# Kernel optimization log

Measured on AMD Instinct MI355X. Metric: run time of the kernel, lower is better.

The kernel has to match this reference:

```python
import jax, jax.numpy as jnp
import numpy as np

D_MODEL, N_LEVELS, N_HEADS, N_POINTS = 256, 3, 8, 2
HEAD_DIM = D_MODEL // N_HEADS
SPATIAL_SHAPES = np.array([[100, 100], [50, 50], [25, 25]], dtype=np.int32)
LEN_IN = int((SPATIAL_SHAPES[:, 0] * SPATIAL_SHAPES[:, 1]).sum())  # 13125
BS, NQ = 16, 900


def setup_inputs() -> dict:
    key = jax.random.key(0)
    ks = jax.random.split(key, 12)
    s = 1.0 / np.sqrt(D_MODEL)
    return {
        "query": jax.random.normal(ks[0], (BS, NQ, N_LEVELS, D_MODEL), jnp.float32),
        "reference_points": jax.random.uniform(ks[1], (BS, NQ, N_LEVELS, 2), jnp.float32),
        "input_flatten": jax.random.normal(ks[2], (BS, LEN_IN, D_MODEL), jnp.float32),
        "input_spatial_shapes": jnp.asarray(SPATIAL_SHAPES),
        "W_value": jax.random.normal(ks[3], (D_MODEL, D_MODEL), jnp.float32) * s,
        "b_value": jnp.zeros((D_MODEL,), jnp.float32),
        "W_off": jax.random.normal(ks[4], (D_MODEL, N_HEADS * N_LEVELS * N_POINTS * 2), jnp.float32) * s * 0.1,
        "b_off": jax.random.normal(ks[5], (N_HEADS * N_LEVELS * N_POINTS * 2,), jnp.float32) * 0.5,
        "W_attn": jax.random.normal(ks[6], (D_MODEL, N_HEADS * N_LEVELS * N_POINTS), jnp.float32) * s,
        "b_attn": jnp.zeros((N_HEADS * N_LEVELS * N_POINTS,), jnp.float32),
        "W_out": jax.random.normal(ks[7], (D_MODEL, D_MODEL), jnp.float32) * s,
        "b_out": jnp.zeros((D_MODEL,), jnp.float32),
    }


def _bilinear_sample(v, loc, H, W):
    """v: (bs, nh, H*W, hd); loc in [0,1]: (bs, nh, N, 2). Zero-pad out of range."""
    hd = v.shape[-1]
    x = loc[..., 0] * W - 0.5
    y = loc[..., 1] * H - 0.5
    x0 = jnp.floor(x)
    y0 = jnp.floor(y)
    out = jnp.zeros(x.shape + (hd,), v.dtype)
    for dx in (0, 1):
        for dy in (0, 1):
            xi = x0 + dx
            yi = y0 + dy
            wgt = (1.0 - jnp.abs(x - xi)) * (1.0 - jnp.abs(y - yi))
            valid = (xi >= 0) & (xi <= W - 1) & (yi >= 0) & (yi <= H - 1)
            xi_c = jnp.clip(xi, 0, W - 1).astype(jnp.int32)
            yi_c = jnp.clip(yi, 0, H - 1).astype(jnp.int32)
            idx = yi_c * W + xi_c  # (bs, nh, N)
            idx = jnp.broadcast_to(idx[..., None], idx.shape + (hd,))
            g = jnp.take_along_axis(v, idx, axis=2)  # (bs, nh, N, hd)
            out = out + g * (wgt * valid.astype(wgt.dtype))[..., None]
    return out


def reference(query, reference_points, input_flatten, input_spatial_shapes,
              W_value, b_value, W_off, b_off, W_attn, b_attn, W_out, b_out):
    bs, nq, fl, _ = query.shape
    shapes = np.asarray(input_spatial_shapes)  # static pyramid shapes

    # value projection: (bs, Len, nh, hd)
    value = (input_flatten @ W_value + b_value).reshape(bs, -1, N_HEADS, HEAD_DIM)

    # sampling offsets: (bs, nq, fl, nh, nl, np, 2)
    offsets = (query @ W_off + b_off).reshape(bs, nq, fl, N_HEADS, N_LEVELS, N_POINTS, 2)
    # attention weights softmax over (nl*np): (bs, nq, fl, nh, nl, np)
    attn = (query @ W_attn + b_attn).reshape(bs, nq, fl, N_HEADS, N_LEVELS * N_POINTS)
    attn = jax.nn.softmax(attn, axis=-1).reshape(bs, nq, fl, N_HEADS, N_LEVELS, N_POINTS)

    # normalized sampling locations: ref + offset / (W_l, H_l)
    normalizer = jnp.asarray(shapes[:, ::-1], jnp.float32)  # (nl, 2) = (W, H)
    loc = reference_points[:, :, :, None, None, None, :] + offsets / normalizer[None, None, None, None, :, None, :]

    splits = np.cumsum([h * w for h, w in shapes])[:-1]
    value_list = jnp.split(value, splits, axis=1)

    out = jnp.zeros((bs, N_HEADS, nq, fl, HEAD_DIM), value.dtype)
    for lvl, (H, W) in enumerate(shapes):
        H, W = int(H), int(W)
        v = jnp.transpose(value_list[lvl], (0, 2, 1, 3))  # (bs, nh, H*W, hd)
        loc_l = jnp.transpose(loc[:, :, :, :, lvl], (0, 3, 1, 2, 4, 5))  # (bs, nh, nq, fl, np, 2)
        loc_flat = loc_l.reshape(bs, N_HEADS, nq * fl * N_POINTS, 2)
        sampled = _bilinear_sample(v, loc_flat, H, W).reshape(bs, N_HEADS, nq, fl, N_POINTS, HEAD_DIM)
        w = jnp.transpose(attn[:, :, :, :, lvl], (0, 3, 1, 2, 4))  # (bs, nh, nq, fl, np)
        out = out + jnp.einsum("bhqfpd,bhqfp->bhqfd", sampled, w)

    out = jnp.transpose(out, (0, 2, 3, 1, 4)).reshape(bs, nq, fl, D_MODEL)
    return out @ W_out + b_out
```

## Files before the change

kernel.cpp:

```cpp
#include <hip/hip_runtime.h>
#include <math.h>

#define D_MODEL   256
#define N_HEADS   8
#define HEAD_DIM  32
#define N_LEVELS  3
#define N_POINTS  2
#define BS        16
#define NQ        900
#define LEN_IN    13125
#define M_Q       (BS * NQ * N_LEVELS)
#define M_V       (BS * LEN_IN)

typedef _Float16 f16x8 __attribute__((ext_vector_type(8)));
typedef _Float16 f16x4 __attribute__((ext_vector_type(4)));
typedef float f32x4 __attribute__((ext_vector_type(4)));

__global__ __launch_bounds__(256) void convert_weight_kernel(
    const float* __restrict__ W, _Float16* __restrict__ Wth,
    _Float16* __restrict__ Wtl, int N, int Npad) {
  const int idx = blockIdx.x * 256 + threadIdx.x;
  if (idx >= Npad * 256) return;
  const int n = idx >> 8;
  const int k = idx & 255;
  const float v = (n < N) ? W[(size_t)k * N + n] : 0.0f;
  const _Float16 h = (_Float16)v;
  Wth[idx] = h;
  Wtl[idx] = (_Float16)(v - (float)h);
}

template <int BN>
__global__ __launch_bounds__(256) void gemm_mfma_f16x3_kernel(
    const float* __restrict__ A, const _Float16* __restrict__ Bth,
    const _Float16* __restrict__ Btl, const float* __restrict__ bias,
    float* __restrict__ C, int M, int N) {
  constexpr int K = 256;
  constexpr int BK = 32;
  constexpr int FC = BN / 64;
  __shared__ _Float16 Ah[64][40];
  __shared__ _Float16 Al[64][40];
  __shared__ _Float16 Bh[BN][40];
  __shared__ _Float16 Bl[BN][40];

  const int tid = threadIdx.x;
  const int wid = tid >> 6;
  const int lane = tid & 63;
  const int bm = blockIdx.x * 64;

  const int a_row0 = tid >> 3;
  const int a_k4 = (tid & 7) * 4;

  f32x4 acc[4][FC];
#pragma unroll
  for (int fr = 0; fr < 4; ++fr)
#pragma unroll
    for (int fc = 0; fc < FC; ++fc) acc[fr][fc] = (f32x4)0.0f;

  const int khi = (lane >> 4) * 8;
  const int rsel = lane & 15;

  for (int k0 = 0; k0 < K; k0 += BK) {
#pragma unroll
    for (int it = 0; it < 2; ++it) {
      const int row = a_row0 + it * 32;
      float4 v = make_float4(0.f, 0.f, 0.f, 0.f);
      if (bm + row < M)
        v = *reinterpret_cast<const float4*>(
            &A[(size_t)(bm + row) * K + k0 + a_k4]);
      f16x4 h, l;
      h[0] = (_Float16)v.x; l[0] = (_Float16)(v.x - (float)h[0]);
      h[1] = (_Float16)v.y; l[1] = (_Float16)(v.y - (float)h[1]);
      h[2] = (_Float16)v.z; l[2] = (_Float16)(v.z - (float)h[2]);
      h[3] = (_Float16)v.w; l[3] = (_Float16)(v.w - (float)h[3]);
      *reinterpret_cast<f16x4*>(&Ah[row][a_k4]) = h;
      *reinterpret_cast<f16x4*>(&Al[row][a_k4]) = l;
    }
#pragma unroll
    for (int it = 0; it < BN / 64; ++it) {
      const int i = tid + 256 * it;
      const int col = i >> 2;
      const int k8 = (i & 3) * 8;
      *reinterpret_cast<f16x8*>(&Bh[col][k8]) =
          *reinterpret_cast<const f16x8*>(&Bth[(size_t)col * K + k0 + k8]);
      *reinterpret_cast<f16x8*>(&Bl[col][k8]) =
          *reinterpret_cast<const f16x8*>(&Btl[(size_t)col * K + k0 + k8]);
    }
    __syncthreads();

    f16x8 afh[4], afl[4], bfh[FC], bfl[FC];
#pragma unroll
    for (int fr = 0; fr < 4; ++fr) {
      afh[fr] = *reinterpret_cast<const f16x8*>(&Ah[fr * 16 + rsel][khi]);
      afl[fr] = *reinterpret_cast<const f16x8*>(&Al[fr * 16 + rsel][khi]);
    }
#pragma unroll
    for (int fc = 0; fc < FC; ++fc) {
      const int c = wid * (BN / 4) + fc * 16 + rsel;
      bfh[fc] = *reinterpret_cast<const f16x8*>(&Bh[c][khi]);
      bfl[fc] = *reinterpret_cast<const f16x8*>(&Bl[c][khi]);
    }
#pragma unroll
    for (int fr = 0; fr < 4; ++fr)
#pragma unroll
      for (int fc = 0; fc < FC; ++fc) {
        acc[fr][fc] = __builtin_amdgcn_mfma_f32_16x16x32_f16(
            afh[fr], bfh[fc], acc[fr][fc], 0, 0, 0);
        acc[fr][fc] = __builtin_amdgcn_mfma_f32_16x16x32_f16(
            afh[fr], bfl[fc], acc[fr][fc], 0, 0, 0);
        acc[fr][fc] = __builtin_amdgcn_mfma_f32_16x16x32_f16(
            afl[fr], bfh[fc], acc[fr][fc], 0, 0, 0);
      }
    __syncthreads();
  }

#pragma unroll
  for (int fr = 0; fr < 4; ++fr) {
#pragma unroll
    for (int i = 0; i < 4; ++i) {
      const int row = bm + fr * 16 + (lane >> 4) * 4 + i;
      if (row >= M) continue;
#pragma unroll
      for (int fc = 0; fc < FC; ++fc) {
        const int col = wid * (BN / 4) + fc * 16 + rsel;
        if (col < N)
          C[(size_t)row * N + col] = acc[fr][fc][i] + bias[col];
      }
    }
  }
}

__global__ __launch_bounds__(256) void sample_kernel(
    const float* __restrict__ value, const float* __restrict__ refpts,
    const float* __restrict__ offs, const float* __restrict__ attn,
    float* __restrict__ out_mid) {
  const int row = blockIdx.x;
  const int tid = threadIdx.x;
  const int h = tid >> 5;
  const int d = tid & 31;
  const int b = row / (NQ * N_LEVELS);

  const int LVL_W[3] = {100, 50, 25};
  const int LVL_H[3] = {100, 50, 25};
  const int LVL_BASE[3] = {0, 10000, 12500};

  const float* off_p  = offs + (size_t)row * 96 + h * 12;
  const float* attn_p = attn + (size_t)row * 48 + h * 6;

  float aw[6];
  float mx = -INFINITY;
#pragma unroll
  for (int j = 0; j < 6; ++j) {
    aw[j] = attn_p[j];
    mx = fmaxf(mx, aw[j]);
  }
  float ssum = 0.f;
#pragma unroll
  for (int j = 0; j < 6; ++j) {
    aw[j] = expf(aw[j] - mx);
    ssum += aw[j];
  }
  const float rs = 1.0f / ssum;

  const float rx = refpts[(size_t)row * 2 + 0];
  const float ry = refpts[(size_t)row * 2 + 1];

  const float* vbase = value + (size_t)b * LEN_IN * 256 + h * 32 + d;
  float acc = 0.f;

#pragma unroll
  for (int l = 0; l < N_LEVELS; ++l) {
    const int W = LVL_W[l], base = LVL_BASE[l];
    const float fW = (float)LVL_W[l], fH = (float)LVL_H[l];
#pragma unroll
    for (int p = 0; p < N_POINTS; ++p) {
      const float ox = off_p[(l * 2 + p) * 2 + 0];
      const float oy = off_p[(l * 2 + p) * 2 + 1];
      const float x = (rx + ox / fW) * fW - 0.5f;
      const float y = (ry + oy / fH) * fH - 0.5f;
      const float x0 = floorf(x);
      const float y0 = floorf(y);
      const float wa = aw[l * 2 + p] * rs;
#pragma unroll
      for (int dy = 0; dy < 2; ++dy) {
#pragma unroll
        for (int dx = 0; dx < 2; ++dx) {
          const float xi = x0 + (float)dx;
          const float yi = y0 + (float)dy;
          const float wgt = (1.0f - fabsf(x - xi)) * (1.0f - fabsf(y - yi));
          const bool valid = (xi >= 0.f) && (xi <= fW - 1.f) &&
                             (yi >= 0.f) && (yi <= fH - 1.f);
          const int xic = (int)fminf(fmaxf(xi, 0.f), fW - 1.f);
          const int yic = (int)fminf(fmaxf(yi, 0.f), fH - 1.f);
          const int pos = base + yic * W + xic;
          const float g = vbase[(size_t)pos * 256];
          acc = fmaf(g, valid ? wgt * wa : 0.0f, acc);
        }
      }
    }
  }
  out_mid[(size_t)row * 256 + tid] = acc;
}

extern "C" void kernel_launch(void* const* d_in, const int* in_sizes, int n_in,
                              void* d_out, int out_size, void* d_ws,
                              size_t ws_size, hipStream_t stream) {
  const float* query   = (const float*)d_in[0];
  const float* refpts  = (const float*)d_in[1];
  const float* in_flat = (const float*)d_in[2];
  const float* W_value = (const float*)d_in[4];
  const float* b_value = (const float*)d_in[5];
  const float* W_off   = (const float*)d_in[6];
  const float* b_off   = (const float*)d_in[7];
  const float* W_attn  = (const float*)d_in[8];
  const float* b_attn  = (const float*)d_in[9];
  const float* W_out   = (const float*)d_in[10];
  const float* b_out   = (const float*)d_in[11];
  float* out = (float*)d_out;

  char* ws = (char*)d_ws;
  float* value   = (float*)ws; ws += (size_t)M_V * 256 * sizeof(float);
  float* out_mid = (float*)ws; ws += (size_t)M_Q * 256 * sizeof(float);
  float* offs    = (float*)ws; ws += (size_t)M_Q * 96 * sizeof(float);
  float* attn    = (float*)ws; ws += (size_t)M_Q * 48 * sizeof(float);
  _Float16* Wvh = (_Float16*)ws; ws += 256 * 256 * sizeof(_Float16);
  _Float16* Wvl = (_Float16*)ws; ws += 256 * 256 * sizeof(_Float16);
  _Float16* Woh = (_Float16*)ws; ws += 256 * 256 * sizeof(_Float16);
  _Float16* Wol = (_Float16*)ws; ws += 256 * 256 * sizeof(_Float16);
  _Float16* Wfh = (_Float16*)ws; ws += 128 * 256 * sizeof(_Float16);
  _Float16* Wfl = (_Float16*)ws; ws += 128 * 256 * sizeof(_Float16);
  _Float16* Wah = (_Float16*)ws; ws += 128 * 256 * sizeof(_Float16);
  _Float16* Wal = (_Float16*)ws; ws += 128 * 256 * sizeof(_Float16);

  const dim3 blk(256);

  convert_weight_kernel<<<dim3(256), blk, 0, stream>>>(W_value, Wvh, Wvl, 256, 256);
  convert_weight_kernel<<<dim3(256), blk, 0, stream>>>(W_out,   Woh, Wol, 256, 256);
  convert_weight_kernel<<<dim3(128), blk, 0, stream>>>(W_off,   Wfh, Wfl,  96, 128);
  convert_weight_kernel<<<dim3(128), blk, 0, stream>>>(W_attn,  Wah, Wal,  48, 128);

  gemm_mfma_f16x3_kernel<256>
      <<<dim3((M_V + 63) / 64), blk, 0, stream>>>(
          in_flat, Wvh, Wvl, b_value, value, M_V, 256);

  gemm_mfma_f16x3_kernel<128>
      <<<dim3((M_Q + 63) / 64), blk, 0, stream>>>(
          query, Wfh, Wfl, b_off, offs, M_Q, 96);

  gemm_mfma_f16x3_kernel<128>
      <<<dim3((M_Q + 63) / 64), blk, 0, stream>>>(
          query, Wah, Wal, b_attn, attn, M_Q, 48);

  sample_kernel<<<dim3(M_Q), blk, 0, stream>>>(value, refpts, offs, attn,
                                               out_mid);

  gemm_mfma_f16x3_kernel<256>
      <<<dim3((M_Q + 63) / 64), blk, 0, stream>>>(
          out_mid, Woh, Wol, b_out, out, M_Q, 256);
}
```

Baseline: 807.8 us.

## Double-buffer A tiles, read B fragments from global, fuse offset/attn GEMMs

```diff
diff --git a/kernel.cpp b/kernel.cpp
--- a/kernel.cpp
+++ b/kernel.cpp
@@ -11,6 +11,8 @@
 #define LEN_IN    13125
 #define M_Q       (BS * NQ * N_LEVELS)
 #define M_V       (BS * LEN_IN)
+#define NCAT      144
+#define NCATP     192
 
 typedef _Float16 f16x8 __attribute__((ext_vector_type(8)));
 typedef _Float16 f16x4 __attribute__((ext_vector_type(4)));
@@ -29,26 +31,50 @@
   Wtl[idx] = (_Float16)(v - (float)h);
 }
 
-template <int BN>
-__global__ __launch_bounds__(256) void gemm_mfma_f16x3_kernel(
+__global__ __launch_bounds__(256) void convert_cat_kernel(
+    const float* __restrict__ Woff, const float* __restrict__ Wattn,
+    const float* __restrict__ boff, const float* __restrict__ battn,
+    _Float16* __restrict__ Wth, _Float16* __restrict__ Wtl,
+    float* __restrict__ bcat) {
+  const int idx = blockIdx.x * 256 + threadIdx.x;
+  if (idx >= NCATP * 256) return;
+  const int n = idx >> 8;
+  const int k = idx & 255;
+  float v = 0.0f;
+  if (n < 96) v = Woff[(size_t)k * 96 + n];
+  else if (n < NCAT) v = Wattn[(size_t)k * 48 + (n - 96)];
+  const _Float16 h = (_Float16)v;
+  Wth[idx] = h;
+  Wtl[idx] = (_Float16)(v - (float)h);
+  if (idx < NCAT) bcat[idx] = (idx < 96) ? boff[idx] : battn[idx - 96];
+}
+
+template <int FC>
+__global__ __launch_bounds__(256) void gemm2_kernel(
     const float* __restrict__ A, const _Float16* __restrict__ Bth,
     const _Float16* __restrict__ Btl, const float* __restrict__ bias,
     float* __restrict__ C, int M, int N) {
   constexpr int K = 256;
-  constexpr int BK = 32;
-  constexpr int FC = BN / 64;
-  __shared__ _Float16 Ah[64][40];
-  __shared__ _Float16 Al[64][40];
-  __shared__ _Float16 Bh[BN][40];
-  __shared__ _Float16 Bl[BN][40];
+  constexpr int LDA = 40;
+  __shared__ _Float16 Ah[2][64][LDA];
+  __shared__ _Float16 Al[2][64][LDA];
 
   const int tid = threadIdx.x;
   const int wid = tid >> 6;
   const int lane = tid & 63;
   const int bm = blockIdx.x * 64;
-
-  const int a_row0 = tid >> 3;
-  const int a_k4 = (tid & 7) * 4;
+  const int rsel = lane & 15;
+  const int khi = (lane >> 4) * 8;
+
+  const int arow = tid >> 3;
+  const int ak = (tid & 7) * 4;
+  const bool g0 = (bm + arow) < M;
+  const bool g1 = (bm + arow + 32) < M;
+  const float* ap0 = A + (size_t)(bm + arow) * K + ak;
+  const float* ap1 = ap0 + (size_t)32 * K;
+
+  const _Float16* bhp = Bth + (size_t)(wid * FC * 16 + rsel) * K + khi;
+  const _Float16* blp = Btl + (size_t)(wid * FC * 16 + rsel) * K + khi;
 
   f32x4 acc[4][FC];
 #pragma unroll
@@ -56,83 +82,110 @@
 #pragma unroll
     for (int fc = 0; fc < FC; ++fc) acc[fr][fc] = (f32x4)0.0f;
 
-  const int khi = (lane >> 4) * 8;
-  const int rsel = lane & 15;
-
-  for (int k0 = 0; k0 < K; k0 += BK) {
-#pragma unroll
-    for (int it = 0; it < 2; ++it) {
-      const int row = a_row0 + it * 32;
-      float4 v = make_float4(0.f, 0.f, 0.f, 0.f);
-      if (bm + row < M)
-        v = *reinterpret_cast<const float4*>(
-            &A[(size_t)(bm + row) * K + k0 + a_k4]);
-      f16x4 h, l;
-      h[0] = (_Float16)v.x; l[0] = (_Float16)(v.x - (float)h[0]);
-      h[1] = (_Float16)v.y; l[1] = (_Float16)(v.y - (float)h[1]);
-      h[2] = (_Float16)v.z; l[2] = (_Float16)(v.z - (float)h[2]);
-      h[3] = (_Float16)v.w; l[3] = (_Float16)(v.w - (float)h[3]);
-      *reinterpret_cast<f16x4*>(&Ah[row][a_k4]) = h;
-      *reinterpret_cast<f16x4*>(&Al[row][a_k4]) = l;
-    }
-#pragma unroll
-    for (int it = 0; it < BN / 64; ++it) {
-      const int i = tid + 256 * it;
-      const int col = i >> 2;
-      const int k8 = (i & 3) * 8;
-      *reinterpret_cast<f16x8*>(&Bh[col][k8]) =
-          *reinterpret_cast<const f16x8*>(&Bth[(size_t)col * K + k0 + k8]);
-      *reinterpret_cast<f16x8*>(&Bl[col][k8]) =
-          *reinterpret_cast<const f16x8*>(&Btl[(size_t)col * K + k0 + k8]);
-    }
-    __syncthreads();
-
-    f16x8 afh[4], afl[4], bfh[FC], bfl[FC];
+  const float4 z4 = make_float4(0.f, 0.f, 0.f, 0.f);
+
+  float4 a0 = g0 ? *reinterpret_cast<const float4*>(ap0) : z4;
+  float4 a1 = g1 ? *reinterpret_cast<const float4*>(ap1) : z4;
+  f16x8 bh[FC], bl[FC];
+#pragma unroll
+  for (int fc = 0; fc < FC; ++fc) {
+    bh[fc] = *reinterpret_cast<const f16x8*>(bhp + (size_t)fc * 16 * K);
+    bl[fc] = *reinterpret_cast<const f16x8*>(blp + (size_t)fc * 16 * K);
+  }
+  {
+    f16x4 h0, l0, h1, l1;
+    h0[0] = (_Float16)a0.x; l0[0] = (_Float16)(a0.x - (float)h0[0]);
+    h0[1] = (_Float16)a0.y; l0[1] = (_Float16)(a0.y - (float)h0[1]);
+    h0[2] = (_Float16)a0.z; l0[2] = (_Float16)(a0.z - (float)h0[2]);
+    h0[3] = (_Float16)a0.w; l0[3] = (_Float16)(a0.w - (float)h0[3]);
+    h1[0] = (_Float16)a1.x; l1[0] = (_Float16)(a1.x - (float)h1[0]);
+    h1[1] = (_Float16)a1.y; l1[1] = (_Float16)(a1.y - (float)h1[1]);
+    h1[2] = (_Float16)a1.z; l1[2] = (_Float16)(a1.z - (float)h1[2]);
+    h1[3] = (_Float16)a1.w; l1[3] = (_Float16)(a1.w - (float)h1[3]);
+    *reinterpret_cast<f16x4*>(&Ah[0][arow][ak]) = h0;
+    *reinterpret_cast<f16x4*>(&Al[0][arow][ak]) = l0;
+    *reinterpret_cast<f16x4*>(&Ah[0][arow + 32][ak]) = h1;
+    *reinterpret_cast<f16x4*>(&Al[0][arow + 32][ak]) = l1;
+  }
+  __syncthreads();
+
+#pragma unroll 2
+  for (int s = 0; s < 8; ++s) {
+    const int cur = s & 1;
+    float4 na0 = z4, na1 = z4;
+    f16x8 nbh[FC], nbl[FC];
+    if (s < 7) {
+      na0 = g0 ? *reinterpret_cast<const float4*>(ap0 + (s + 1) * 32) : z4;
+      na1 = g1 ? *reinterpret_cast<const float4*>(ap1 + (s + 1) * 32) : z4;
+#pragma unroll
+      for (int fc = 0; fc < FC; ++fc) {
+        nbh[fc] = *reinterpret_cast<const f16x8*>(
+            bhp + (size_t)fc * 16 * K + (s + 1) * 32);
+        nbl[fc] = *reinterpret_cast<const f16x8*>(
+            blp + (size_t)fc * 16 * K + (s + 1) * 32);
+      }
+    }
+    f16x8 afh[4], afl[4];
 #pragma unroll
     for (int fr = 0; fr < 4; ++fr) {
-      afh[fr] = *reinterpret_cast<const f16x8*>(&Ah[fr * 16 + rsel][khi]);
-      afl[fr] = *reinterpret_cast<const f16x8*>(&Al[fr * 16 + rsel][khi]);
-    }
-#pragma unroll
-    for (int fc = 0; fc < FC; ++fc) {
-      const int c = wid * (BN / 4) + fc * 16 + rsel;
-      bfh[fc] = *reinterpret_cast<const f16x8*>(&Bh[c][khi]);
-      bfl[fc] = *reinterpret_cast<const f16x8*>(&Bl[c][khi]);
+      afh[fr] = *reinterpret_cast<const f16x8*>(&Ah[cur][fr * 16 + rsel][khi]);
+      afl[fr] = *reinterpret_cast<const f16x8*>(&Al[cur][fr * 16 + rsel][khi]);
     }
 #pragma unroll
     for (int fr = 0; fr < 4; ++fr)
 #pragma unroll
       for (int fc = 0; fc < FC; ++fc) {
         acc[fr][fc] = __builtin_amdgcn_mfma_f32_16x16x32_f16(
-            afh[fr], bfh[fc], acc[fr][fc], 0, 0, 0);
+            afh[fr], bh[fc], acc[fr][fc], 0, 0, 0);
         acc[fr][fc] = __builtin_amdgcn_mfma_f32_16x16x32_f16(
-            afh[fr], bfl[fc], acc[fr][fc], 0, 0, 0);
+            afh[fr], bl[fc], acc[fr][fc], 0, 0, 0);
         acc[fr][fc] = __builtin_amdgcn_mfma_f32_16x16x32_f16(
-            afl[fr], bfh[fc], acc[fr][fc], 0, 0, 0);
+            afl[fr], bh[fc], acc[fr][fc], 0, 0, 0);
       }
-    __syncthreads();
-  }
-
-#pragma unroll
-  for (int fr = 0; fr < 4; ++fr) {
+    if (s < 7) {
+      const int nxt = cur ^ 1;
+      f16x4 h0, l0, h1, l1;
+      h0[0] = (_Float16)na0.x; l0[0] = (_Float16)(na0.x - (float)h0[0]);
+      h0[1] = (_Float16)na0.y; l0[1] = (_Float16)(na0.y - (float)h0[1]);
+      h0[2] = (_Float16)na0.z; l0[2] = (_Float16)(na0.z - (float)h0[2]);
+      h0[3] = (_Float16)na0.w; l0[3] = (_Float16)(na0.w - (float)h0[3]);
+      h1[0] = (_Float16)na1.x; l1[0] = (_Float16)(na1.x - (float)h1[0]);
+      h1[1] = (_Float16)na1.y; l1[1] = (_Float16)(na1.y - (float)h1[1]);
+      h1[2] = (_Float16)na1.z; l1[2] = (_Float16)(na1.z - (float)h1[2]);
+      h1[3] = (_Float16)na1.w; l1[3] = (_Float16)(na1.w - (float)h1[3]);
+      *reinterpret_cast<f16x4*>(&Ah[nxt][arow][ak]) = h0;
+      *reinterpret_cast<f16x4*>(&Al[nxt][arow][ak]) = l0;
+      *reinterpret_cast<f16x4*>(&Ah[nxt][arow + 32][ak]) = h1;
+      *reinterpret_cast<f16x4*>(&Al[nxt][arow + 32][ak]) = l1;
+#pragma unroll
+      for (int fc = 0; fc < FC; ++fc) { bh[fc] = nbh[fc]; bl[fc] = nbl[fc]; }
+      __syncthreads();
+    }
+  }
+
+  float bs_[FC];
+#pragma unroll
+  for (int fc = 0; fc < FC; ++fc) {
+    const int col = wid * FC * 16 + fc * 16 + rsel;
+    bs_[fc] = (col < N) ? bias[col] : 0.0f;
+  }
+#pragma unroll
+  for (int fr = 0; fr < 4; ++fr)
 #pragma unroll
     for (int i = 0; i < 4; ++i) {
       const int row = bm + fr * 16 + (lane >> 4) * 4 + i;
       if (row >= M) continue;
 #pragma unroll
       for (int fc = 0; fc < FC; ++fc) {
-        const int col = wid * (BN / 4) + fc * 16 + rsel;
-        if (col < N)
-          C[(size_t)row * N + col] = acc[fr][fc][i] + bias[col];
+        const int col = wid * FC * 16 + fc * 16 + rsel;
+        if (col < N) C[(size_t)row * N + col] = acc[fr][fc][i] + bs_[fc];
       }
     }
-  }
 }
 
 __global__ __launch_bounds__(256) void sample_kernel(
     const float* __restrict__ value, const float* __restrict__ refpts,
-    const float* __restrict__ offs, const float* __restrict__ attn,
-    float* __restrict__ out_mid) {
+    const float* __restrict__ offs_attn, float* __restrict__ out_mid) {
   const int row = blockIdx.x;
   const int tid = threadIdx.x;
   const int h = tid >> 5;
@@ -143,8 +196,8 @@
   const int LVL_H[3] = {100, 50, 25};
   const int LVL_BASE[3] = {0, 10000, 12500};
 
-  const float* off_p  = offs + (size_t)row * 96 + h * 12;
-  const float* attn_p = attn + (size_t)row * 48 + h * 6;
+  const float* off_p  = offs_attn + (size_t)row * NCAT + h * 12;
+  const float* attn_p = offs_attn + (size_t)row * NCAT + 96 + h * 6;
 
   float aw[6];
   float mx = -INFINITY;
@@ -218,42 +271,33 @@
   float* out = (float*)d_out;
 
   char* ws = (char*)d_ws;
-  float* value   = (float*)ws; ws += (size_t)M_V * 256 * sizeof(float);
-  float* out_mid = (float*)ws; ws += (size_t)M_Q * 256 * sizeof(float);
-  float* offs    = (float*)ws; ws += (size_t)M_Q * 96 * sizeof(float);
-  float* attn    = (float*)ws; ws += (size_t)M_Q * 48 * sizeof(float);
+  float* value     = (float*)ws; ws += (size_t)M_V * 256 * sizeof(float);
+  float* out_mid   = (float*)ws; ws += (size_t)M_Q * 256 * sizeof(float);
+  float* offs_attn = (float*)ws; ws += (size_t)M_Q * NCAT * sizeof(float);
   _Float16* Wvh = (_Float16*)ws; ws += 256 * 256 * sizeof(_Float16);
   _Float16* Wvl = (_Float16*)ws; ws += 256 * 256 * sizeof(_Float16);
   _Float16* Woh = (_Float16*)ws; ws += 256 * 256 * sizeof(_Float16);
   _Float16* Wol = (_Float16*)ws; ws += 256 * 256 * sizeof(_Float16);
-  _Float16* Wfh = (_Float16*)ws; ws += 128 * 256 * sizeof(_Float16);
-  _Float16* Wfl = (_Float16*)ws; ws += 128 * 256 * sizeof(_Float16);
-  _Float16* Wah = (_Float16*)ws; ws += 128 * 256 * sizeof(_Float16);
-  _Float16* Wal = (_Float16*)ws; ws += 128 * 256 * sizeof(_Float16);
+  _Float16* Wch = (_Float16*)ws; ws += NCATP * 256 * sizeof(_Float16);
+  _Float16* Wcl = (_Float16*)ws; ws += NCATP * 256 * sizeof(_Float16);
+  float* bcat   = (float*)ws;    ws += 256 * sizeof(float);
 
   const dim3 blk(256);
 
   convert_weight_kernel<<<dim3(256), blk, 0, stream>>>(W_value, Wvh, Wvl, 256, 256);
   convert_weight_kernel<<<dim3(256), blk, 0, stream>>>(W_out,   Woh, Wol, 256, 256);
-  convert_weight_kernel<<<dim3(128), blk, 0, stream>>>(W_off,   Wfh, Wfl,  96, 128);
-  convert_weight_kernel<<<dim3(128), blk, 0, stream>>>(W_attn,  Wah, Wal,  48, 128);
-
-  gemm_mfma_f16x3_kernel<256>
-      <<<dim3((M_V + 63) / 64), blk, 0, stream>>>(
-          in_flat, Wvh, Wvl, b_value, value, M_V, 256);
-
-  gemm_mfma_f16x3_kernel<128>
-      <<<dim3((M_Q + 63) / 64), blk, 0, stream>>>(
-          query, Wfh, Wfl, b_off, offs, M_Q, 96);
-
-  gemm_mfma_f16x3_kernel<128>
-      <<<dim3((M_Q + 63) / 64), blk, 0, stream>>>(
-          query, Wah, Wal, b_attn, attn, M_Q, 48);
-
-  sample_kernel<<<dim3(M_Q), blk, 0, stream>>>(value, refpts, offs, attn,
+  convert_cat_kernel<<<dim3(NCATP), blk, 0, stream>>>(W_off, W_attn, b_off, b_attn,
+                                                      Wch, Wcl, bcat);
+
+  gemm2_kernel<4><<<dim3((M_V + 63) / 64), blk, 0, stream>>>(
+      in_flat, Wvh, Wvl, b_value, value, M_V, 256);
+
+  gemm2_kernel<3><<<dim3((M_Q + 63) / 64), blk, 0, stream>>>(
+      query, Wch, Wcl, bcat, offs_attn, M_Q, NCAT);
+
+  sample_kernel<<<dim3(M_Q), blk, 0, stream>>>(value, refpts, offs_attn,
                                                out_mid);
 
-  gemm_mfma_f16x3_kernel<256>
-      <<<dim3((M_Q + 63) / 64), blk, 0, stream>>>(
-          out_mid, Woh, Wol, b_out, out, M_Q, 256);
-}
+  gemm2_kernel<4><<<dim3((M_Q + 63) / 64), blk, 0, stream>>>(
+      out_mid, Woh, Wol, b_out, out, M_Q, 256);
+}
```

After: 810.6 us. No clear change (+0.3%).
